# Kernel tuning notes

Hardware: AMD Instinct MI355X
Metric: run time of the kernel (lower is better)

## Reference

```python
import jax, jax.numpy as jnp
import numpy as np

NUM_MIX = 50
CMD_LEN = 4
ARG_LEN = 6
MIX_TEMP = 0.0001
GAUSS_TEMP = 0.0001


def setup_inputs() -> dict:
    key = jax.random.key(0)
    k1, k2, k3 = jax.random.split(key, 3)
    S, B, H = 51, 2048, 1024
    out_ch = CMD_LEN + ARG_LEN * NUM_MIX * 3  # 904
    decoder_output = jax.random.normal(k1, (S, B, H), dtype=jnp.float32)
    W = jax.random.normal(k2, (out_ch, H), dtype=jnp.float32) * (1.0 / np.sqrt(H))
    b = jax.random.normal(k3, (out_ch,), dtype=jnp.float32) * 0.01
    return {"decoder_output": decoder_output, "W": W, "b": b}


def reference(decoder_output, W, b):
    S, B, H = decoder_output.shape
    # fc: [S,B,H] @ [H,out_ch] + b  -> [S,B,904]
    ret = jnp.einsum('sbh,oh->sbo', decoder_output, W) + b

    key = jax.random.key(42)
    k_cmd, k_mix, k_gauss = jax.random.split(key, 3)

    # command: temperature softmax + categorical sample + one-hot
    cmd_logits = ret[..., :CMD_LEN] / MIX_TEMP  # [S,B,4]
    cmd_idx = jax.random.categorical(k_cmd, cmd_logits)  # [S,B]
    command = jax.nn.one_hot(cmd_idx, CMD_LEN, dtype=decoder_output.dtype)

    # MDN coefficients over flattened rows: N = S*B*ARG_LEN
    arguments = ret[..., CMD_LEN:].reshape(-1, 3 * NUM_MIX)  # [N,150]
    logmix = arguments[:, :NUM_MIX]
    mean = arguments[:, NUM_MIX:2 * NUM_MIX]
    logstd = arguments[:, 2 * NUM_MIX:]
    logmix = logmix - jax.nn.logsumexp(logmix, axis=-1, keepdims=True)

    # sample mixture component with temperature (softmax of logmix/temp)
    mix_idx = jax.random.categorical(k_mix, logmix / MIX_TEMP)  # [N]

    # vectorized gather of chosen mean/logstd (replaces per-row python loop)
    chosen_mean = jnp.take_along_axis(mean, mix_idx[:, None], axis=1)[:, 0]
    chosen_logstd = jnp.take_along_axis(logstd, mix_idx[:, None], axis=1)[:, 0]

    noise = jax.random.normal(k_gauss, chosen_mean.shape, dtype=chosen_mean.dtype)
    noise = noise * np.sqrt(GAUSS_TEMP)
    args_out = chosen_mean + jnp.exp(chosen_logstd) * noise  # [N]
    args_out = args_out.reshape(-1, B, ARG_LEN)  # [S,B,6]

    return jnp.concatenate([command, args_out], axis=-1)  # [S,B,10]
```

## Files before the change

### kernel.cpp

```cpp
#include <hip/hip_runtime.h>
#include <stdint.h>
#include <math.h>

#pragma clang fp contract(off)

#define M_TOTAL 104448
#define N_OUT   904
#define K_DIM   1024

#define BM 64
#define BN 64
#define BK 16

typedef float f32x2 __attribute__((ext_vector_type(2)));

__device__ inline f32x2 pk_mul(f32x2 a, f32x2 b) {
    f32x2 d;
    asm("v_pk_mul_f32 %0, %1, %2" : "=v"(d) : "v"(a), "v"(b));
    return d;
}
__device__ inline f32x2 pk_add(f32x2 a, f32x2 b) {
    f32x2 d;
    asm("v_pk_add_f32 %0, %1, %2" : "=v"(d) : "v"(a), "v"(b));
    return d;
}

__host__ __device__ inline uint32_t rotl32(uint32_t x, int r) {
    return (x << r) | (x >> (32 - r));
}

__host__ __device__ inline void threefry2x32(uint32_t k0, uint32_t k1,
                                             uint32_t x0, uint32_t x1,
                                             uint32_t& o0, uint32_t& o1) {
    uint32_t ks2 = k0 ^ k1 ^ 0x1BD11BDAu;
    x0 += k0; x1 += k1;
#define R4(a,b,c,d) \
    x0 += x1; x1 = rotl32(x1,(a)); x1 ^= x0; \
    x0 += x1; x1 = rotl32(x1,(b)); x1 ^= x0; \
    x0 += x1; x1 = rotl32(x1,(c)); x1 ^= x0; \
    x0 += x1; x1 = rotl32(x1,(d)); x1 ^= x0;
    R4(13,15,26,6)  x0 += k1;  x1 += ks2 + 1u;
    R4(17,29,16,24) x0 += ks2; x1 += k0  + 2u;
    R4(13,15,26,6)  x0 += k0;  x1 += k1  + 3u;
    R4(17,29,16,24) x0 += k1;  x1 += ks2 + 4u;
    R4(13,15,26,6)  x0 += ks2; x1 += k0  + 5u;
#undef R4
    o0 = x0; o1 = x1;
}

__device__ inline uint32_t random_bits_part(uint32_t k0, uint32_t k1, uint32_t idx) {
    uint32_t o0, o1;
    threefry2x32(k0, k1, 0u, idx, o0, o1);
    return o0 ^ o1;
}

__device__ inline float bits_to_unit(uint32_t bits) {
    return __uint_as_float((bits >> 9) | 0x3f800000u) - 1.0f;
}

__device__ inline float logf_cr(float x) { return (float)log((double)x); }
__device__ inline float expf_cr(float x) { return (float)exp((double)x); }

__device__ inline float gumbel_at(uint32_t k0, uint32_t k1, uint32_t idx) {
    float f = bits_to_unit(random_bits_part(k0, k1, idx));
    float u = fmaxf(f, 1.17549435e-38f);
    float t = logf_cr(u);
    return -logf_cr(-t);
}

__device__ inline float erfinv_xla(float x) {
    float w = -log1pf(-x * x);
    float p;
    if (w < 5.0f) {
        w = w - 2.5f;
        p = 2.81022636e-08f;
        p = 3.43273939e-07f  + p * w;
        p = -3.5233877e-06f  + p * w;
        p = -4.39150654e-06f + p * w;
        p = 0.00021858087f   + p * w;
        p = -0.00125372503f  + p * w;
        p = -0.00417768164f  + p * w;
        p = 0.246640727f     + p * w;
        p = 1.50140941f      + p * w;
    } else {
        w = sqrtf(w) - 3.0f;
        p = -0.000200214257f;
        p = 0.000100950558f  + p * w;
        p = 0.00134934322f   + p * w;
        p = -0.00367342844f  + p * w;
        p = 0.00573950773f   + p * w;
        p = -0.0076224613f   + p * w;
        p = 0.00943887047f   + p * w;
        p = 1.00167406f      + p * w;
        p = 2.83297682f      + p * w;
    }
    return p * x;
}

__global__ __launch_bounds__(256) void gemm_np_sse_pk(
    const float* __restrict__ X,
    const float* __restrict__ W,
    const float* __restrict__ bias,
    float* __restrict__ ret,
    int rows)
{
    __shared__ f32x2 As2[BK / 2][BM];
    __shared__ f32x2 Bs2[BK / 2][BN];

    const int t  = threadIdx.x;
    const int tx = t & 15;
    const int ty = t >> 4;
    const int m0 = blockIdx.y * BM;
    const int n0 = blockIdx.x * BN;

    const int sm  = t >> 2;
    const int skq = t & 3;
    const int smw = sm ^ (skq << 2);

    f32x2 acc[2][4][4];
#pragma unroll
    for (int h = 0; h < 2; h++)
#pragma unroll
        for (int i = 0; i < 4; i++)
#pragma unroll
            for (int j = 0; j < 4; j++) acc[h][i][j] = (f32x2){0.0f, 0.0f};

    for (int k0 = 0; k0 < K_DIM; k0 += BK) {
        float4 av = *(const float4*)(X + (size_t)(m0 + sm) * K_DIM + k0 + skq * 4);
        float4 bv;
        int gn = n0 + sm;
        if (gn < N_OUT) bv = *(const float4*)(W + (size_t)gn * K_DIM + k0 + skq * 4);
        else            bv = make_float4(0.f, 0.f, 0.f, 0.f);

        __syncthreads();
        As2[skq * 2 + 0][smw] = (f32x2){av.x, av.y};
        As2[skq * 2 + 1][smw] = (f32x2){av.z, av.w};
        Bs2[skq * 2 + 0][smw] = (f32x2){bv.x, bv.y};
        Bs2[skq * 2 + 1][smw] = (f32x2){bv.z, bv.w};
        __syncthreads();

#pragma unroll
        for (int q = 3; q >= 0; q--) {
#pragma unroll
            for (int half = 0; half < 2; half++) {
                const int kp = q * 2 + half;
                const int sw = q << 2;
                const f32x2* aP = &As2[kp][(ty * 4) ^ sw];
                const f32x2* bP = &Bs2[kp][(tx * 4) ^ sw];
                f32x2 a0 = aP[0], a1 = aP[1], a2 = aP[2], a3 = aP[3];
                f32x2 b0 = bP[0], b1 = bP[1], b2 = bP[2], b3 = bP[3];
                acc[half][0][0] = pk_add(pk_mul(a0, b0), acc[half][0][0]);
                acc[half][0][1] = pk_add(pk_mul(a0, b1), acc[half][0][1]);
                acc[half][0][2] = pk_add(pk_mul(a0, b2), acc[half][0][2]);
                acc[half][0][3] = pk_add(pk_mul(a0, b3), acc[half][0][3]);
                acc[half][1][0] = pk_add(pk_mul(a1, b0), acc[half][1][0]);
                acc[half][1][1] = pk_add(pk_mul(a1, b1), acc[half][1][1]);
                acc[half][1][2] = pk_add(pk_mul(a1, b2), acc[half][1][2]);
                acc[half][1][3] = pk_add(pk_mul(a1, b3), acc[half][1][3]);
                acc[half][2][0] = pk_add(pk_mul(a2, b0), acc[half][2][0]);
                acc[half][2][1] = pk_add(pk_mul(a2, b1), acc[half][2][1]);
                acc[half][2][2] = pk_add(pk_mul(a2, b2), acc[half][2][2]);
                acc[half][2][3] = pk_add(pk_mul(a2, b3), acc[half][2][3]);
                acc[half][3][0] = pk_add(pk_mul(a3, b0), acc[half][3][0]);
                acc[half][3][1] = pk_add(pk_mul(a3, b1), acc[half][3][1]);
                acc[half][3][2] = pk_add(pk_mul(a3, b2), acc[half][3][2]);
                acc[half][3][3] = pk_add(pk_mul(a3, b3), acc[half][3][3]);
            }
        }
    }

#pragma unroll
    for (int i = 0; i < 4; i++) {
        int m = m0 + ty * 4 + i;
        if (m >= rows) continue;
#pragma unroll
        for (int j = 0; j < 4; j++) {
            int o = n0 + tx * 4 + j;
            if (o >= N_OUT) continue;
            f32x2 s01 = acc[0][i][j];
            f32x2 s23 = acc[1][i][j];
            float res = (s01.x + s01.y) + (s23.x + s23.y);
            ret[(size_t)m * N_OUT + o] = res + bias[o];
        }
    }
}

__global__ __launch_bounds__(256) void sample_kernel(
    const float* __restrict__ ret,
    float* __restrict__ out,
    int m0_global, int rows,
    uint32_t kc0, uint32_t kc1,
    uint32_t km0, uint32_t km1,
    uint32_t kg0, uint32_t kg1)
{
    const int lane = threadIdx.x & 63;
    const int wid  = threadIdx.x >> 6;
    const int rloc = blockIdx.x * 4 + wid;
    if (rloc >= rows) return;
    const int m = m0_global + rloc;

    const float* r = ret + (size_t)rloc * N_OUT;
    float* o = out + (size_t)m * 10;

    const float LO = __uint_as_float(0xBF7FFFFFu);
    const float SQRT2 = __uint_as_float(0x3FB504F3u);

    {
        float v; int idx = lane;
        if (lane < 4) {
            float g = gumbel_at(kc0, kc1, (uint32_t)(m * 4 + lane));
            v = r[lane] / 0.0001f + g;
        } else {
            v = -INFINITY;
        }
#pragma unroll
        for (int off = 1; off < 64; off <<= 1) {
            float v2 = __shfl_xor(v, off);
            int   i2 = __shfl_xor(idx, off);
            if (v2 > v || (v2 == v && i2 < idx)) { v = v2; idx = i2; }
        }
        if (lane < 4) o[lane] = (lane == idx) ? 1.0f : 0.0f;
    }

    for (int a = 0; a < 6; a++) {
        const float* base = r + 4 + a * 150;
        float l = (lane < 50) ? base[lane] : -INFINITY;

        float mx = l;
#pragma unroll
        for (int off = 1; off < 64; off <<= 1) mx = fmaxf(mx, __shfl_xor(mx, off));

        float e = (lane < 50) ? expf_cr(l - mx) : 0.0f;

        float rj = (lane < 8) ? e : 0.0f;
#pragma unroll
        for (int tstep = 1; tstep <= 5; tstep++) {
            float ev = __shfl(e, (lane & 7) + 8 * tstep);
            if (lane < 8) rj = rj + ev;
        }
        float r0 = __shfl(rj, 0), r1 = __shfl(rj, 1), r2 = __shfl(rj, 2), r3 = __shfl(rj, 3);
        float r4 = __shfl(rj, 4), r5 = __shfl(rj, 5), r6 = __shfl(rj, 6), r7 = __shfl(rj, 7);
        float s = ((r0 + r1) + (r2 + r3)) + ((r4 + r5) + (r6 + r7));
        s = s + __shfl(e, 48);
        s = s + __shfl(e, 49);

        float lse = logf_cr(s) + mx;

        float vv; int ii = lane;
        if (lane < 50) {
            float g = gumbel_at(km0, km1, (uint32_t)((m * 6 + a) * 50 + lane));
            vv = (l - lse) / 0.0001f + g;
        } else {
            vv = -INFINITY;
        }
#pragma unroll
        for (int off = 1; off < 64; off <<= 1) {
            float v2 = __shfl_xor(vv, off);
            int   i2 = __shfl_xor(ii, off);
            if (v2 > vv || (v2 == vv && i2 < ii)) { vv = v2; ii = i2; }
        }

        if (lane == 0) {
            float mean = base[50 + ii];
            float lstd = base[100 + ii];
            uint32_t eidx = (uint32_t)(m * 6 + a);
            float f = bits_to_unit(random_bits_part(kg0, kg1, eidx));
            float val = f * 2.0f + LO;
            val = fmaxf(LO, val);
            float nrm = SQRT2 * erfinv_xla(val);
            float noise = nrm * 0.01f;
            o[4 + a] = mean + expf_cr(lstd) * noise;
        }
    }
}

extern "C" void kernel_launch(void* const* d_in, const int* in_sizes, int n_in,
                              void* d_out, int out_size, void* d_ws, size_t ws_size,
                              hipStream_t stream) {
    const float* X    = (const float*)d_in[0];
    const float* W    = (const float*)d_in[1];
    const float* bias = (const float*)d_in[2];
    float* out = (float*)d_out;
    float* ws  = (float*)d_ws;

    uint32_t kc0, kc1, km0, km1, kg0, kg1;
    threefry2x32(0u, 42u, 0u, 0u, kc0, kc1);
    threefry2x32(0u, 42u, 0u, 1u, km0, km1);
    threefry2x32(0u, 42u, 0u, 2u, kg0, kg1);

    const size_t rowBytes = (size_t)N_OUT * sizeof(float);
    size_t rowsCap = ws_size / rowBytes;
    int chunk = (rowsCap >= (size_t)M_TOTAL) ? M_TOTAL : (int)rowsCap;
    chunk -= chunk % BM;
    if (chunk <= 0) chunk = BM;

    const int gx = (N_OUT + BN - 1) / BN;

    for (int m0 = 0; m0 < M_TOTAL; m0 += chunk) {
        int rows = M_TOTAL - m0;
        if (rows > chunk) rows = chunk;
        dim3 ggrid(gx, rows / BM);
        gemm_np_sse_pk<<<ggrid, 256, 0, stream>>>(X + (size_t)m0 * K_DIM, W, bias, ws, rows);
        sample_kernel<<<dim3(rows / 4), 256, 0, stream>>>(ws, out, m0, rows,
                                                          kc0, kc1, km0, km1, kg0, kg1);
    }
}
```

Measured before the change: 4.939 ms.

## Load A tile directly into registers with double-buffered prefetch, enlarge BM

The GEMM no longer stages the X tile in shared memory. Each thread now loads eight rows of A straight from global memory into registers, double-buffered so the next k-slice is prefetched while the current one is computed. The block tile grows to 128 rows, only W goes through a padded shared buffer, and launch bounds ask for 2 blocks per SU. This removes A-side LDS traffic and raises arithmetic intensity per thread, but it adds register pressure and uncoalesced per-thread row loads of X.

Result: slower. 5.829 ms (+18.0%).

```diff
diff --git a/kernel.cpp b/kernel.cpp
--- a/kernel.cpp
+++ b/kernel.cpp
@@ -8,9 +8,10 @@
 #define N_OUT   904
 #define K_DIM   1024
 
-#define BM 64
+#define BM 128
 #define BN 64
 #define BK 16
+#define MR 8
 
 typedef float f32x2 __attribute__((ext_vector_type(2)));
 
@@ -97,15 +98,14 @@
     return p * x;
 }
 
-__global__ __launch_bounds__(256) void gemm_np_sse_pk(
+__global__ __launch_bounds__(256, 2) void gemm_np_sse_rA(
     const float* __restrict__ X,
     const float* __restrict__ W,
     const float* __restrict__ bias,
     float* __restrict__ ret,
     int rows)
 {
-    __shared__ f32x2 As2[BK / 2][BM];
-    __shared__ f32x2 Bs2[BK / 2][BN];
+    __shared__ float4 Bs[4 * 82];
 
     const int t  = threadIdx.x;
     const int tx = t & 15;
@@ -113,65 +113,76 @@
     const int m0 = blockIdx.y * BM;
     const int n0 = blockIdx.x * BN;
 
-    const int sm  = t >> 2;
+    const int sn  = t >> 2;
     const int skq = t & 3;
-    const int smw = sm ^ (skq << 2);
-
-    f32x2 acc[2][4][4];
+
+    const float* Abase = X + (size_t)(m0 + ty * MR) * K_DIM;
+    const float* Wrow  = W + (size_t)(n0 + sn) * K_DIM + skq * 4;
+    const bool   wok   = (n0 + sn) < N_OUT;
+    const int    bst   = skq * 82 + sn + (sn >> 2);
+    const int    bbase = tx * 5;
+
+    f32x2 acc[2][MR][4];
 #pragma unroll
     for (int h = 0; h < 2; h++)
 #pragma unroll
-        for (int i = 0; i < 4; i++)
+        for (int i = 0; i < MR; i++)
 #pragma unroll
             for (int j = 0; j < 4; j++) acc[h][i][j] = (f32x2){0.0f, 0.0f};
 
+    float4 A0[MR], A1[MR];
+
+#pragma unroll
+    for (int i = 0; i < MR; i++)
+        A1[i] = *(const float4*)(Abase + i * K_DIM + 12);
+
+#define LOAD_A(BUF, KOFF)                                              \
+    do { int _ko = (KOFF);                                             \
+        if (_ko < K_DIM) {                                             \
+            _Pragma("unroll")                                          \
+            for (int i = 0; i < MR; i++)                               \
+                BUF[i] = *(const float4*)(Abase + i * K_DIM + _ko);    \
+        }                                                              \
+    } while (0)
+
+#define COMPUTE(BUF, Q)                                                \
+    do {                                                               \
+        float4 b0 = Bs[(Q) * 82 + bbase + 0];                          \
+        float4 b1 = Bs[(Q) * 82 + bbase + 1];                          \
+        float4 b2 = Bs[(Q) * 82 + bbase + 2];                          \
+        float4 b3 = Bs[(Q) * 82 + bbase + 3];                          \
+        f32x2 b01[4] = {{b0.x,b0.y},{b1.x,b1.y},{b2.x,b2.y},{b3.x,b3.y}}; \
+        f32x2 b23[4] = {{b0.z,b0.w},{b1.z,b1.w},{b2.z,b2.w},{b3.z,b3.w}}; \
+        _Pragma("unroll")                                              \
+        for (int i = 0; i < MR; i++) {                                 \
+            f32x2 a01 = {BUF[i].x, BUF[i].y};                          \
+            f32x2 a23 = {BUF[i].z, BUF[i].w};                          \
+            _Pragma("unroll")                                          \
+            for (int j = 0; j < 4; j++) {                              \
+                acc[0][i][j] = pk_add(pk_mul(a01, b01[j]), acc[0][i][j]); \
+                acc[1][i][j] = pk_add(pk_mul(a23, b23[j]), acc[1][i][j]); \
+            }                                                          \
+        }                                                              \
+    } while (0)
+
     for (int k0 = 0; k0 < K_DIM; k0 += BK) {
-        float4 av = *(const float4*)(X + (size_t)(m0 + sm) * K_DIM + k0 + skq * 4);
-        float4 bv;
-        int gn = n0 + sm;
-        if (gn < N_OUT) bv = *(const float4*)(W + (size_t)gn * K_DIM + k0 + skq * 4);
-        else            bv = make_float4(0.f, 0.f, 0.f, 0.f);
-
+        float4 wv = wok ? *(const float4*)(Wrow + k0)
+                        : make_float4(0.f, 0.f, 0.f, 0.f);
         __syncthreads();
-        As2[skq * 2 + 0][smw] = (f32x2){av.x, av.y};
-        As2[skq * 2 + 1][smw] = (f32x2){av.z, av.w};
-        Bs2[skq * 2 + 0][smw] = (f32x2){bv.x, bv.y};
-        Bs2[skq * 2 + 1][smw] = (f32x2){bv.z, bv.w};
+        Bs[bst] = wv;
         __syncthreads();
 
-#pragma unroll
-        for (int q = 3; q >= 0; q--) {
-#pragma unroll
-            for (int half = 0; half < 2; half++) {
-                const int kp = q * 2 + half;
-                const int sw = q << 2;
-                const f32x2* aP = &As2[kp][(ty * 4) ^ sw];
-                const f32x2* bP = &Bs2[kp][(tx * 4) ^ sw];
-                f32x2 a0 = aP[0], a1 = aP[1], a2 = aP[2], a3 = aP[3];
-                f32x2 b0 = bP[0], b1 = bP[1], b2 = bP[2], b3 = bP[3];
-                acc[half][0][0] = pk_add(pk_mul(a0, b0), acc[half][0][0]);
-                acc[half][0][1] = pk_add(pk_mul(a0, b1), acc[half][0][1]);
-                acc[half][0][2] = pk_add(pk_mul(a0, b2), acc[half][0][2]);
-                acc[half][0][3] = pk_add(pk_mul(a0, b3), acc[half][0][3]);
-                acc[half][1][0] = pk_add(pk_mul(a1, b0), acc[half][1][0]);
-                acc[half][1][1] = pk_add(pk_mul(a1, b1), acc[half][1][1]);
-                acc[half][1][2] = pk_add(pk_mul(a1, b2), acc[half][1][2]);
-                acc[half][1][3] = pk_add(pk_mul(a1, b3), acc[half][1][3]);
-                acc[half][2][0] = pk_add(pk_mul(a2, b0), acc[half][2][0]);
-                acc[half][2][1] = pk_add(pk_mul(a2, b1), acc[half][2][1]);
-                acc[half][2][2] = pk_add(pk_mul(a2, b2), acc[half][2][2]);
-                acc[half][2][3] = pk_add(pk_mul(a2, b3), acc[half][2][3]);
-                acc[half][3][0] = pk_add(pk_mul(a3, b0), acc[half][3][0]);
-                acc[half][3][1] = pk_add(pk_mul(a3, b1), acc[half][3][1]);
-                acc[half][3][2] = pk_add(pk_mul(a3, b2), acc[half][3][2]);
-                acc[half][3][3] = pk_add(pk_mul(a3, b3), acc[half][3][3]);
-            }
-        }
-    }
-
-#pragma unroll
-    for (int i = 0; i < 4; i++) {
-        int m = m0 + ty * 4 + i;
+        COMPUTE(A1, 3); LOAD_A(A0, k0 + 8);
+        COMPUTE(A0, 2); LOAD_A(A1, k0 + 4);
+        COMPUTE(A1, 1); LOAD_A(A0, k0 + 0);
+        COMPUTE(A0, 0); LOAD_A(A1, k0 + BK + 12);
+    }
+#undef LOAD_A
+#undef COMPUTE
+
+#pragma unroll
+    for (int i = 0; i < MR; i++) {
+        int m = m0 + ty * MR + i;
         if (m >= rows) continue;
 #pragma unroll
         for (int j = 0; j < 4; j++) {
@@ -184,6 +195,7 @@
         }
     }
 }
+
 
 __global__ __launch_bounds__(256) void sample_kernel(
     const float* __restrict__ ret,
@@ -300,7 +312,7 @@
         int rows = M_TOTAL - m0;
         if (rows > chunk) rows = chunk;
         dim3 ggrid(gx, rows / BM);
-        gemm_np_sse_pk<<<ggrid, 256, 0, stream>>>(X + (size_t)m0 * K_DIM, W, bias, ws, rows);
+        gemm_np_sse_rA<<<ggrid, 256, 0, stream>>>(X + (size_t)m0 * K_DIM, W, bias, ws, rows);
         sample_kernel<<<dim3(rows / 4), 256, 0, stream>>>(ws, out, m0, rows,
                                                           kc0, kc1, km0, km1, kg0, kg1);
     }
```

## Prefetch next K tile into registers and pad LDS for 128-bit reads

Applied to the files above, without the earlier changes.

The GEMM kernel now loads the next K-slice of X and W into registers while the current tile is being computed, so global loads overlap the FMA work instead of stalling before each tile. The XOR swizzle on shared memory is replaced by padding: the A tile keeps a plain layout and the B tile uses a strided padded index. This lets inner-loop operands be read as float4 pairs rather than individual f32x2 loads. The cost is more registers for the prefetched values and a larger shared footprint, and bank conflicts may behave differently under the new layout.

New measurement: 4.918 ms. About the same (-0.4%).

```diff
diff --git a/kernel.cpp b/kernel.cpp
--- a/kernel.cpp
+++ b/kernel.cpp
@@ -97,15 +97,15 @@
     return p * x;
 }
 
-__global__ __launch_bounds__(256) void gemm_np_sse_pk(
+__global__ __launch_bounds__(256) void gemm_np_sse_pk2(
     const float* __restrict__ X,
     const float* __restrict__ W,
     const float* __restrict__ bias,
     float* __restrict__ ret,
     int rows)
 {
-    __shared__ f32x2 As2[BK / 2][BM];
-    __shared__ f32x2 Bs2[BK / 2][BN];
+    __shared__ f32x2 As2[8][68];
+    __shared__ f32x2 Bs2[8][100];
 
     const int t  = threadIdx.x;
     const int tx = t & 15;
@@ -115,7 +115,11 @@
 
     const int sm  = t >> 2;
     const int skq = t & 3;
-    const int smw = sm ^ (skq << 2);
+    const int bse = sm + 2 * (sm >> 2);
+
+    const float* Xrow = X + (size_t)(m0 + sm) * K_DIM + skq * 4;
+    const float* Wrow = W + (size_t)(n0 + sm) * K_DIM + skq * 4;
+    const bool   wok  = (n0 + sm) < N_OUT;
 
     f32x2 acc[2][4][4];
 #pragma unroll
@@ -125,46 +129,52 @@
 #pragma unroll
             for (int j = 0; j < 4; j++) acc[h][i][j] = (f32x2){0.0f, 0.0f};
 
+    float4 av = *(const float4*)(Xrow);
+    float4 bv = wok ? *(const float4*)(Wrow) : make_float4(0.f, 0.f, 0.f, 0.f);
+
     for (int k0 = 0; k0 < K_DIM; k0 += BK) {
-        float4 av = *(const float4*)(X + (size_t)(m0 + sm) * K_DIM + k0 + skq * 4);
-        float4 bv;
-        int gn = n0 + sm;
-        if (gn < N_OUT) bv = *(const float4*)(W + (size_t)gn * K_DIM + k0 + skq * 4);
-        else            bv = make_float4(0.f, 0.f, 0.f, 0.f);
-
         __syncthreads();
-        As2[skq * 2 + 0][smw] = (f32x2){av.x, av.y};
-        As2[skq * 2 + 1][smw] = (f32x2){av.z, av.w};
-        Bs2[skq * 2 + 0][smw] = (f32x2){bv.x, bv.y};
-        Bs2[skq * 2 + 1][smw] = (f32x2){bv.z, bv.w};
+        As2[skq * 2 + 0][sm]  = (f32x2){av.x, av.y};
+        As2[skq * 2 + 1][sm]  = (f32x2){av.z, av.w};
+        Bs2[skq * 2 + 0][bse] = (f32x2){bv.x, bv.y};
+        Bs2[skq * 2 + 1][bse] = (f32x2){bv.z, bv.w};
         __syncthreads();
 
+        if (k0 + BK < K_DIM) {
+            av = *(const float4*)(Xrow + k0 + BK);
+            bv = wok ? *(const float4*)(Wrow + k0 + BK)
+                     : make_float4(0.f, 0.f, 0.f, 0.f);
+        }
+
 #pragma unroll
         for (int q = 3; q >= 0; q--) {
 #pragma unroll
-            for (int half = 0; half < 2; half++) {
-                const int kp = q * 2 + half;
-                const int sw = q << 2;
-                const f32x2* aP = &As2[kp][(ty * 4) ^ sw];
-                const f32x2* bP = &Bs2[kp][(tx * 4) ^ sw];
-                f32x2 a0 = aP[0], a1 = aP[1], a2 = aP[2], a3 = aP[3];
-                f32x2 b0 = bP[0], b1 = bP[1], b2 = bP[2], b3 = bP[3];
-                acc[half][0][0] = pk_add(pk_mul(a0, b0), acc[half][0][0]);
-                acc[half][0][1] = pk_add(pk_mul(a0, b1), acc[half][0][1]);
-                acc[half][0][2] = pk_add(pk_mul(a0, b2), acc[half][0][2]);
-                acc[half][0][3] = pk_add(pk_mul(a0, b3), acc[half][0][3]);
-                acc[half][1][0] = pk_add(pk_mul(a1, b0), acc[half][1][0]);
-                acc[half][1][1] = pk_add(pk_mul(a1, b1), acc[half][1][1]);
-                acc[half][1][2] = pk_add(pk_mul(a1, b2), acc[half][1][2]);
-                acc[half][1][3] = pk_add(pk_mul(a1, b3), acc[half][1][3]);
-                acc[half][2][0] = pk_add(pk_mul(a2, b0), acc[half][2][0]);
-                acc[half][2][1] = pk_add(pk_mul(a2, b1), acc[half][2][1]);
-                acc[half][2][2] = pk_add(pk_mul(a2, b2), acc[half][2][2]);
-                acc[half][2][3] = pk_add(pk_mul(a2, b3), acc[half][2][3]);
-                acc[half][3][0] = pk_add(pk_mul(a3, b0), acc[half][3][0]);
-                acc[half][3][1] = pk_add(pk_mul(a3, b1), acc[half][3][1]);
-                acc[half][3][2] = pk_add(pk_mul(a3, b2), acc[half][3][2]);
-                acc[half][3][3] = pk_add(pk_mul(a3, b3), acc[half][3][3]);
+            for (int h = 0; h < 2; h++) {
+                const int kp = q * 2 + h;
+                float4 aa0 = *(const float4*)&As2[kp][ty * 4];
+                float4 aa1 = *(const float4*)&As2[kp][ty * 4 + 2];
+                float4 bb0 = *(const float4*)&Bs2[kp][tx * 6];
+                float4 bb1 = *(const float4*)&Bs2[kp][tx * 6 + 2];
+                f32x2 a0 = {aa0.x, aa0.y}, a1 = {aa0.z, aa0.w};
+                f32x2 a2 = {aa1.x, aa1.y}, a3 = {aa1.z, aa1.w};
+                f32x2 b0 = {bb0.x, bb0.y}, b1 = {bb0.z, bb0.w};
+                f32x2 b2 = {bb1.x, bb1.y}, b3 = {bb1.z, bb1.w};
+                acc[h][0][0] = pk_add(pk_mul(a0, b0), acc[h][0][0]);
+                acc[h][0][1] = pk_add(pk_mul(a0, b1), acc[h][0][1]);
+                acc[h][0][2] = pk_add(pk_mul(a0, b2), acc[h][0][2]);
+                acc[h][0][3] = pk_add(pk_mul(a0, b3), acc[h][0][3]);
+                acc[h][1][0] = pk_add(pk_mul(a1, b0), acc[h][1][0]);
+                acc[h][1][1] = pk_add(pk_mul(a1, b1), acc[h][1][1]);
+                acc[h][1][2] = pk_add(pk_mul(a1, b2), acc[h][1][2]);
+                acc[h][1][3] = pk_add(pk_mul(a1, b3), acc[h][1][3]);
+                acc[h][2][0] = pk_add(pk_mul(a2, b0), acc[h][2][0]);
+                acc[h][2][1] = pk_add(pk_mul(a2, b1), acc[h][2][1]);
+                acc[h][2][2] = pk_add(pk_mul(a2, b2), acc[h][2][2]);
+                acc[h][2][3] = pk_add(pk_mul(a2, b3), acc[h][2][3]);
+                acc[h][3][0] = pk_add(pk_mul(a3, b0), acc[h][3][0]);
+                acc[h][3][1] = pk_add(pk_mul(a3, b1), acc[h][3][1]);
+                acc[h][3][2] = pk_add(pk_mul(a3, b2), acc[h][3][2]);
+                acc[h][3][3] = pk_add(pk_mul(a3, b3), acc[h][3][3]);
             }
         }
     }
@@ -300,7 +310,7 @@
         int rows = M_TOTAL - m0;
         if (rows > chunk) rows = chunk;
         dim3 ggrid(gx, rows / BM);
-        gemm_np_sse_pk<<<ggrid, 256, 0, stream>>>(X + (size_t)m0 * K_DIM, W, bias, ws, rows);
+        gemm_np_sse_pk2<<<ggrid, 256, 0, stream>>>(X + (size_t)m0 * K_DIM, W, bias, ws, rows);
         sample_kernel<<<dim3(rows / 4), 256, 0, stream>>>(ws, out, m0, rows,
                                                           kc0, kc1, km0, km1, kg0, kg1);
     }
```
